# Kernel tuning notes

Measured on AMD Instinct MI355X. Metric: run time of the kernel, lower is better.

Reference implementation:

```python
import jax, jax.numpy as jnp
import numpy as np

T, B, DIN, DH, NH = 256, 256, 1024, 1024, 16
HD = DH // NH


def setup_inputs() -> dict:
    key = jax.random.key(0)
    ks = jax.random.split(key, 11)
    w = lambda k, shape: jax.random.normal(k, shape, jnp.float32) * 0.02
    return {
        "inputs": jax.random.normal(ks[0], (T, B, DIN), jnp.float32),
        "Wg": w(ks[1], (4, DIN + DH, DH)),  # forget, input, update, output pre-gate linears
        "bg": w(ks[2], (4, DH)),
        "Wq": w(ks[3], (3, DH, DH)),  # forget, input, output attention gates
        "bq": w(ks[4], (3, DH)),
        "Wk": w(ks[5], (3, DH, DH)),
        "bk": w(ks[6], (3, DH)),
        "Wv": w(ks[7], (3, DH, DH)),
        "bv": w(ks[8], (3, DH)),
        "Wo": w(ks[9], (3, DH, DH)),
        "bo": w(ks[10], (3, DH)),
    }


def reference(inputs, Wg, bg, Wq, bq, Wk, bk, Wv, bv, Wo, bo):
    scale = 1.0 / np.sqrt(HD)
    sel = jnp.array([0, 1, 3])  # gates that use attention: forget, input, output

    def attn_gate(x):
        # x: [3, B, DH] -- three gate pre-activations processed in parallel
        q = (jnp.einsum('gbd,gde->gbe', x, Wq) + bq[:, None, :]).reshape(3, B, NH, HD)
        k = (jnp.einsum('gbd,gde->gbe', x, Wk) + bk[:, None, :]).reshape(3, B, NH, HD)
        v = (jnp.einsum('gbd,gde->gbe', x, Wv) + bv[:, None, :]).reshape(3, B, NH, HD)
        # attention ACROSS heads: [3, B, NH, NH]
        aw = jax.nn.softmax(jnp.einsum('gbhd,gbkd->gbhk', q, k) * scale, axis=-1)
        ao = jnp.einsum('gbhk,gbkd->gbhd', aw, v).reshape(3, B, DH)
        return jax.nn.sigmoid(jnp.einsum('gbd,gde->gbe', ao, Wo) + bo[:, None, :])

    def step(carry, x):
        hx, cx = carry
        comb = jnp.concatenate([x, hx], axis=1)          # [B, DIN+DH]
        pre = jnp.einsum('bi,gio->gbo', comb, Wg) + bg[:, None, :]  # [4, B, DH]
        f, i, o = attn_gate(pre[sel])                    # each [B, DH]
        g = jnp.tanh(pre[2])
        cx = f * cx + i * g
        hx = o * jnp.tanh(cx)
        return (hx, cx), hx

    init = (jnp.zeros((B, DH), inputs.dtype), jnp.zeros((B, DH), inputs.dtype))
    (hx, cx), outputs = jax.lax.scan(step, init, inputs)
    return outputs, hx, cx
```

## Files before the change

kernel.cpp:

```cpp
#include <hip/hip_runtime.h>

typedef __attribute__((ext_vector_type(8))) short bf8;
typedef __attribute__((ext_vector_type(8))) unsigned short us8;
typedef __attribute__((ext_vector_type(4))) unsigned short us4;
typedef __attribute__((ext_vector_type(4))) float f4;

#define NB 256
#define OUT_HX_OFF ((size_t)256 * 256 * 1024)
#define OUT_CX_OFF (OUT_HX_OFF + (size_t)256 * 1024)

static __device__ __forceinline__ unsigned short f2bf(float f) {
    unsigned u = __builtin_bit_cast(unsigned, f);
    return (unsigned short)((u + 0x7FFFu + ((u >> 16) & 1u)) >> 16);
}
static __device__ __forceinline__ float bf2f(unsigned short h) {
    return __builtin_bit_cast(float, (unsigned)h << 16);
}
static __device__ __forceinline__ float sigm(float x) {
    return 1.0f / (1.0f + __expf(-x));
}

#define MFMA16(a, b, c) __builtin_amdgcn_mfma_f32_16x16x32_bf16(a, b, c, 0, 0, 0)

#define GLDS16(g, l)                                                        \
    __builtin_amdgcn_global_load_lds(                                       \
        (const __attribute__((address_space(1))) void*)(g),                 \
        (__attribute__((address_space(3))) void*)(l), 16, 0, 0)

#define WAITV(n) asm volatile("s_waitcnt vmcnt(" #n ")" ::: "memory")
#define WAITL0 asm volatile("s_waitcnt lgkmcnt(0)" ::: "memory")
#define BARRIER                                                             \
    do {                                                                    \
        __builtin_amdgcn_s_barrier();                                       \
        __builtin_amdgcn_sched_barrier(0);                                  \
    } while (0)

template <int R>
static __device__ __forceinline__ void stage64(const unsigned short* g, int gstride,
                                               unsigned short* lds, int wave, int lane) {
#pragma unroll
    for (int j = 0; j < R / 32; ++j) {
        const int seg = wave * (R / 32) + j;
        const int row = seg * 8 + (lane >> 3);
        const int chunk = (lane & 7) ^ (row & 7);
        GLDS16(g + (size_t)row * gstride + chunk * 8, lds + seg * 512);
    }
}

static __device__ __forceinline__ bf8 fragld(const unsigned short* lds, int row, int ck) {
    return *(const bf8*)&lds[row * 64 + (((ck) ^ (row & 7)) << 3)];
}

__global__ __launch_bounds__(256) void k_x2bf(const float* __restrict__ src,
                                              unsigned short* __restrict__ dst, int n4) {
    const int stride = gridDim.x * 256;
    for (int i = blockIdx.x * 256 + threadIdx.x; i < n4; i += stride) {
        f4 v = ((const f4*)src)[i];
        us4 o;
        o[0] = f2bf(v[0]); o[1] = f2bf(v[1]); o[2] = f2bf(v[2]); o[3] = f2bf(v[3]);
        ((us4*)dst)[i] = o;
    }
}

__global__ __launch_bounds__(256) void k_transpose(const float* __restrict__ src,
                                                   unsigned short* __restrict__ dst,
                                                   int K, int N) {
    __shared__ float tile[32][33];
    const int tx = threadIdx.x & 31, ty = threadIdx.x >> 5;
    const int n0 = blockIdx.x * 32, k0 = blockIdx.y * 32;
#pragma unroll
    for (int i = 0; i < 4; ++i) tile[ty + i * 8][tx] = src[(size_t)(k0 + ty + i * 8) * N + n0 + tx];
    __syncthreads();
#pragma unroll
    for (int i = 0; i < 4; ++i)
        dst[(size_t)(n0 + ty + i * 8) * K + k0 + tx] = f2bf(tile[tx][ty + i * 8]);
}

__global__ __launch_bounds__(256) void k_wfz(const unsigned short* __restrict__ wqkvT,
                                             const unsigned short* __restrict__ wgnt,
                                             unsigned short* __restrict__ wbigX,
                                             unsigned short* __restrict__ wbigH) {
    __shared__ unsigned short sA[2][128 * 64];
    __shared__ unsigned short sB[2][128 * 64];
    const int tid = threadIdx.x, lane = tid & 63, wave = tid >> 6;
    const int z = blockIdx.z, j = z >> 1, xh = z & 1;
    const int gp = j / 3, which = j % 3;
    const int selg = (gp == 2) ? 3 : gp;
    const unsigned short* Aab = wqkvT + ((size_t)gp * 3072 + which * 1024) * 1024;
    const unsigned short* Bb = wgnt + (size_t)selg * 2048 * 1024 + (size_t)xh * 1024 * 1024;
    unsigned short* outp = (xh ? wbigH : wbigX) + (size_t)j * 1024 * 1024;
    const int n0 = blockIdx.x * 128, m0 = blockIdx.y * 128;
    const int wy = (wave >> 1) * 64, wx = (wave & 1) * 64;
    const int fr = lane & 15, fq = lane >> 4;
    f4 acc[4][4] = {};

    stage64<128>(Aab + (size_t)m0 * 1024, 1024, sA[0], wave, lane);
    stage64<128>(Bb + (size_t)n0 * 1024, 1024, sB[0], wave, lane);
    WAITV(0); BARRIER;
#pragma unroll
    for (int i = 0; i < 16; ++i) {
        if (i + 1 < 16) {
            stage64<128>(Aab + (size_t)m0 * 1024 + (i + 1) * 64, 1024, sA[(i + 1) & 1], wave, lane);
            stage64<128>(Bb + (size_t)n0 * 1024 + (i + 1) * 64, 1024, sB[(i + 1) & 1], wave, lane);
        }
        const unsigned short* A = sA[i & 1];
        const unsigned short* Bm = sB[i & 1];
#pragma unroll
        for (int ks = 0; ks < 2; ++ks) {
            bf8 af[4], bfv[4];
#pragma unroll
            for (int mi = 0; mi < 4; ++mi) af[mi] = fragld(A, wy + mi * 16 + fr, ks * 4 + fq);
#pragma unroll
            for (int ni = 0; ni < 4; ++ni) bfv[ni] = fragld(Bm, wx + ni * 16 + fr, ks * 4 + fq);
#pragma unroll
            for (int mi = 0; mi < 4; ++mi)
#pragma unroll
                for (int ni = 0; ni < 4; ++ni)
                    acc[mi][ni] = MFMA16(af[mi], bfv[ni], acc[mi][ni]);
        }
        if (i + 1 < 16) { WAITL0; WAITV(0); BARRIER; }
    }
#pragma unroll
    for (int mi = 0; mi < 4; ++mi)
#pragma unroll
        for (int ni = 0; ni < 4; ++ni) {
            const int col = n0 + wx + ni * 16 + fr;
#pragma unroll
            for (int j2 = 0; j2 < 4; ++j2) {
                const int row = m0 + wy + mi * 16 + fq * 4 + j2;
                outp[(size_t)row * 1024 + col] = f2bf(acc[mi][ni][j2]);
            }
        }
}

__global__ __launch_bounds__(256) void k_seg9(const unsigned short* __restrict__ wgT,
                                              unsigned short* __restrict__ wbigX,
                                              unsigned short* __restrict__ wbigH) {
    const int d = blockIdx.x, k4 = threadIdx.x * 4;
    us4 vx = *(const us4*)(wgT + (size_t)(2048 + d) * 2048 + k4);
    us4 vh = *(const us4*)(wgT + (size_t)(2048 + d) * 2048 + 1024 + k4);
    *(us4*)(wbigX + (size_t)(9216 + d) * 1024 + k4) = vx;
    *(us4*)(wbigH + (size_t)(9216 + d) * 1024 + k4) = vh;
}

__global__ __launch_bounds__(256) void k_cbig(const float* __restrict__ bg,
                                              const float* __restrict__ Wq,
                                              const float* __restrict__ Wk,
                                              const float* __restrict__ Wv,
                                              const float* __restrict__ bq,
                                              const float* __restrict__ bk,
                                              const float* __restrict__ bv,
                                              float* __restrict__ cbig) {
    const int n = blockIdx.x * 256 + threadIdx.x;
    const int j = n >> 10, d = n & 1023;
    float s;
    if (j < 9) {
        const int gp = j / 3, which = j % 3;
        const int selg = (gp == 2) ? 3 : gp;
        const float* W = which == 0 ? Wq : (which == 1 ? Wk : Wv);
        const float* bqkv = which == 0 ? bq : (which == 1 ? bk : bv);
        s = bqkv[gp * 1024 + d];
        const float* wb = W + (size_t)gp * 1024 * 1024;
        const float* bgb = bg + selg * 1024;
        for (int k = 0; k < 1024; ++k) s += bgb[k] * wb[(size_t)k * 1024 + d];
    } else {
        s = bg[2048 + d];
    }
    cbig[n] = s;
}

__global__ __launch_bounds__(256) void k_xbig(const unsigned short* __restrict__ xbf,
                                              const unsigned short* __restrict__ wbigX,
                                              const float* __restrict__ cbig,
                                              unsigned short* __restrict__ XBIG) {
    __shared__ unsigned short sA[2][128 * 64];
    __shared__ unsigned short sB[2][128 * 64];
    const int tid = threadIdx.x, lane = tid & 63, wave = tid >> 6;
    const int n0 = blockIdx.x * 128;
    const size_t m0 = (size_t)blockIdx.y * 128;
    const int wy = (wave >> 1) * 64, wx = (wave & 1) * 64;
    const int fr = lane & 15, fq = lane >> 4;
    f4 acc[4][4] = {};

    stage64<128>(xbf + m0 * 1024, 1024, sA[0], wave, lane);
    stage64<128>(wbigX + (size_t)n0 * 1024, 1024, sB[0], wave, lane);
    WAITV(0); BARRIER;
#pragma unroll
    for (int i = 0; i < 16; ++i) {
        if (i + 1 < 16) {
            stage64<128>(xbf + m0 * 1024 + (i + 1) * 64, 1024, sA[(i + 1) & 1], wave, lane);
            stage64<128>(wbigX + (size_t)n0 * 1024 + (i + 1) * 64, 1024, sB[(i + 1) & 1], wave, lane);
        }
        const unsigned short* A = sA[i & 1];
        const unsigned short* Bm = sB[i & 1];
#pragma unroll
        for (int ks = 0; ks < 2; ++ks) {
            bf8 af[4], bfv[4];
#pragma unroll
            for (int mi = 0; mi < 4; ++mi) af[mi] = fragld(A, wy + mi * 16 + fr, ks * 4 + fq);
#pragma unroll
            for (int ni = 0; ni < 4; ++ni) bfv[ni] = fragld(Bm, wx + ni * 16 + fr, ks * 4 + fq);
#pragma unroll
            for (int mi = 0; mi < 4; ++mi)
#pragma unroll
                for (int ni = 0; ni < 4; ++ni)
                    acc[mi][ni] = MFMA16(af[mi], bfv[ni], acc[mi][ni]);
        }
        if (i + 1 < 16) { WAITL0; WAITV(0); BARRIER; }
    }
#pragma unroll
    for (int mi = 0; mi < 4; ++mi)
#pragma unroll
        for (int ni = 0; ni < 4; ++ni) {
            const int col = n0 + wx + ni * 16 + fr;
            const float b = cbig[col];
#pragma unroll
            for (int j = 0; j < 4; ++j) {
                const size_t row = m0 + wy + mi * 16 + fq * 4 + j;
                XBIG[row * 10240 + col] = f2bf(acc[mi][ni][j] + b);
            }
        }
}

__global__ __launch_bounds__(256, 3) void k_qg(
    const unsigned short* __restrict__ hxbf,
    const unsigned short* __restrict__ wbigH,
    const unsigned short* __restrict__ XBIGt,
    unsigned short* __restrict__ qkvbf,
    float* __restrict__ gupd) {
    __shared__ unsigned short sA[4][32 * 64];
    __shared__ unsigned short sB[4][64 * 64];
    const int tid = threadIdx.x, lane = tid & 63, wave = tid >> 6;
    const int n0 = blockIdx.x * 64, b0 = blockIdx.y * 32;
    const unsigned short* Aab = hxbf + (size_t)b0 * 1024;
    const unsigned short* Bb = wbigH + (size_t)n0 * 1024;
    const int wr = (wave & 1) * 16, wc = (wave >> 1) * 32;
    const int fr = lane & 15, fq = lane >> 4;
    f4 acc[2] = {};

#pragma unroll
    for (int p = 0; p < 3; ++p) {
        stage64<32>(Aab + p * 64, 1024, sA[p], wave, lane);
        stage64<64>(Bb + p * 64, 1024, sB[p], wave, lane);
    }
    WAITV(6); BARRIER;
#pragma unroll
    for (int i = 0; i < 16; ++i) {
        if (i + 3 < 16) {
            stage64<32>(Aab + (i + 3) * 64, 1024, sA[(i + 3) & 3], wave, lane);
            stage64<64>(Bb + (i + 3) * 64, 1024, sB[(i + 3) & 3], wave, lane);
        }
        const unsigned short* A = sA[i & 3];
        const unsigned short* Bm = sB[i & 3];
#pragma unroll
        for (int ks = 0; ks < 2; ++ks) {
            bf8 a0 = fragld(A, wr + fr, ks * 4 + fq);
            bf8 b0v = fragld(Bm, wc + fr, ks * 4 + fq);
            bf8 b1v = fragld(Bm, wc + 16 + fr, ks * 4 + fq);
            acc[0] = MFMA16(a0, b0v, acc[0]);
            acc[1] = MFMA16(a0, b1v, acc[1]);
        }
        if (i < 15) {
            WAITL0;
            if (i + 3 < 16) { WAITV(6); }
            else if (i + 2 < 16) { WAITV(3); }
            else { WAITV(0); }
            BARRIER;
        }
    }
#pragma unroll
    for (int ni = 0; ni < 2; ++ni) {
        const int col = n0 + wc + ni * 16 + fr;
        const int seg = col >> 10, d = col & 1023;
#pragma unroll
        for (int j = 0; j < 4; ++j) {
            const int row = b0 + wr + fq * 4 + j;
            const float v = acc[ni][j] + bf2f(XBIGt[(size_t)row * 10240 + col]);
            if (seg == 9) {
                gupd[(size_t)row * 1024 + d] = tanhf(v);
            } else {
                const int gp = seg / 3, which = seg % 3;
                qkvbf[((size_t)gp * NB + row) * 3072 + which * 1024 + d] = f2bf(v);
            }
        }
    }
}

__global__ __launch_bounds__(256, 2) void k_pre(
    const unsigned short* __restrict__ hxbf,
    const unsigned short* __restrict__ xt,
    const unsigned short* __restrict__ wgT,
    const float* __restrict__ bg,
    unsigned short* __restrict__ prebf,
    float* __restrict__ gupd) {
    __shared__ unsigned short sA[4][32 * 64];
    __shared__ unsigned short sB[4][64 * 64];
    const int tid = threadIdx.x, lane = tid & 63, wave = tid >> 6;
    const int n0 = blockIdx.x * 64, b0 = blockIdx.y * 32;
    const int wr = (wave & 1) * 16, wc = (wave >> 1) * 32;
    const int fr = lane & 15, fq = lane >> 4;
    constexpr int NT = 32;
    f4 acc[2] = {};

    const unsigned short* hb = hxbf + (size_t)b0 * 1024;
    const unsigned short* xb = xt + (size_t)b0 * 1024;
    auto asrc = [&](int i) -> const unsigned short* {
        return i < 16 ? xb + i * 64 : hb + (i - 16) * 64;
    };
    auto bsrc = [&](int i) -> const unsigned short* {
        return wgT + (size_t)n0 * 2048 + i * 64;
    };

#pragma unroll
    for (int p = 0; p < 3; ++p) {
        stage64<32>(asrc(p), 1024, sA[p], wave, lane);
        stage64<64>(bsrc(p), 2048, sB[p], wave, lane);
    }
    WAITV(6); BARRIER;
#pragma unroll
    for (int i = 0; i < NT; ++i) {
        if (i + 3 < NT) {
            stage64<32>(asrc(i + 3), 1024, sA[(i + 3) & 3], wave, lane);
            stage64<64>(bsrc(i + 3), 2048, sB[(i + 3) & 3], wave, lane);
        }
        const unsigned short* A = sA[i & 3];
        const unsigned short* Bm = sB[i & 3];
#pragma unroll
        for (int ks = 0; ks < 2; ++ks) {
            bf8 a0 = fragld(A, wr + fr, ks * 4 + fq);
            bf8 b0v = fragld(Bm, wc + fr, ks * 4 + fq);
            bf8 b1v = fragld(Bm, wc + 16 + fr, ks * 4 + fq);
            acc[0] = MFMA16(a0, b0v, acc[0]);
            acc[1] = MFMA16(a0, b1v, acc[1]);
        }
        if (i < NT - 1) {
            WAITL0;
            if (i + 3 < NT) { WAITV(6); }
            else if (i + 2 < NT) { WAITV(3); }
            else { WAITV(0); }
            BARRIER;
        }
    }
#pragma unroll
    for (int ni = 0; ni < 2; ++ni) {
        const int col = n0 + wc + ni * 16 + fr;
        const int gg = col >> 10, d = col & 1023;
#pragma unroll
        for (int j = 0; j < 4; ++j) {
            const int row = b0 + wr + fq * 4 + j;
            float v = acc[ni][j] + bg[col];
            if (gg == 2) {
                gupd[(size_t)row * 1024 + d] = tanhf(v);
            } else {
                const int gm = (gg == 3) ? 2 : gg;
                prebf[((size_t)gm * NB + row) * 1024 + d] = f2bf(v);
            }
        }
    }
}

__global__ __launch_bounds__(256, 3) void k_qkv(
    const unsigned short* __restrict__ prebf,
    const unsigned short* __restrict__ wqkvT,
    const float* __restrict__ bq,
    const float* __restrict__ bk,
    const float* __restrict__ bv,
    unsigned short* __restrict__ qkvbf) {
    __shared__ unsigned short sA[4][32 * 64];
    __shared__ unsigned short sB[4][64 * 64];
    const int tid = threadIdx.x, lane = tid & 63, wave = tid >> 6;
    const int g = blockIdx.z;
    const int n0 = blockIdx.x * 64, b0 = blockIdx.y * 32;
    const unsigned short* Aab = prebf + ((size_t)g * NB + b0) * 1024;
    const unsigned short* Bb = wqkvT + ((size_t)g * 3072 + n0) * 1024;
    const int wr = (wave & 1) * 16, wc = (wave >> 1) * 32;
    const int fr = lane & 15, fq = lane >> 4;
    f4 acc[2] = {};

#pragma unroll
    for (int p = 0; p < 3; ++p) {
        stage64<32>(Aab + p * 64, 1024, sA[p], wave, lane);
        stage64<64>(Bb + p * 64, 1024, sB[p], wave, lane);
    }
    WAITV(6); BARRIER;
#pragma unroll
    for (int i = 0; i < 16; ++i) {
        if (i + 3 < 16) {
            stage64<32>(Aab + (i + 3) * 64, 1024, sA[(i + 3) & 3], wave, lane);
            stage64<64>(Bb + (i + 3) * 64, 1024, sB[(i + 3) & 3], wave, lane);
        }
        const unsigned short* A = sA[i & 3];
        const unsigned short* Bm = sB[i & 3];
#pragma unroll
        for (int ks = 0; ks < 2; ++ks) {
            bf8 a0 = fragld(A, wr + fr, ks * 4 + fq);
            bf8 b0v = fragld(Bm, wc + fr, ks * 4 + fq);
            bf8 b1v = fragld(Bm, wc + 16 + fr, ks * 4 + fq);
            acc[0] = MFMA16(a0, b0v, acc[0]);
            acc[1] = MFMA16(a0, b1v, acc[1]);
        }
        if (i < 15) {
            WAITL0;
            if (i + 3 < 16) { WAITV(6); }
            else if (i + 2 < 16) { WAITV(3); }
            else { WAITV(0); }
            BARRIER;
        }
    }
#pragma unroll
    for (int ni = 0; ni < 2; ++ni) {
        const int col = n0 + wc + ni * 16 + fr;
        const int which = col >> 10, d = col & 1023;
        const float* bp = which == 0 ? bq : (which == 1 ? bk : bv);
        const float bias = bp[g * 1024 + d];
#pragma unroll
        for (int j = 0; j < 4; ++j) {
            const int row = b0 + wr + fq * 4 + j;
            qkvbf[((size_t)g * NB + row) * 3072 + col] = f2bf(acc[ni][j] + bias);
        }
    }
}

__global__ __launch_bounds__(256) void k_attn(const unsigned short* __restrict__ qkvbf,
                                              unsigned short* __restrict__ aobf) {
    __shared__ unsigned short qs[16][72], ksm[16][72], vsm[16][72];
    __shared__ float aw[16][17];
    const int b = blockIdx.x, g = blockIdx.y, tid = threadIdx.x;
    const unsigned short* src = qkvbf + ((size_t)g * NB + b) * 3072;
#pragma unroll
    for (int j = 0; j < 3; ++j) {
        const int n = (j * 256 + tid) * 4;
        us4 dv = *(const us4*)(src + n);
        const int part = n >> 10, h = (n >> 6) & 15, c = n & 63;
        unsigned short* dst = part == 0 ? &qs[h][c] : (part == 1 ? &ksm[h][c] : &vsm[h][c]);
        *(us4*)dst = dv;
    }
    __syncthreads();
    const int h = tid >> 4, kp = tid & 15;
    float s = 0.f;
#pragma unroll
    for (int dblk = 0; dblk < 8; ++dblk) {
        us8 qv = *(const us8*)&qs[h][dblk * 8];
        us8 kv = *(const us8*)&ksm[kp][dblk * 8];
#pragma unroll
        for (int e = 0; e < 8; ++e) s += bf2f(qv[e]) * bf2f(kv[e]);
    }
    s *= 0.125f;
    float m = s;
#pragma unroll
    for (int off = 8; off; off >>= 1) m = fmaxf(m, __shfl_xor(m, off, 16));
    const float p = __expf(s - m);
    float sum = p;
#pragma unroll
    for (int off = 8; off; off >>= 1) sum += __shfl_xor(sum, off, 16);
    aw[h][kp] = p / sum;
    __syncthreads();
    float a0 = 0.f, a1 = 0.f, a2 = 0.f, a3 = 0.f;
#pragma unroll
    for (int kk = 0; kk < 16; ++kk) {
        const float w = aw[h][kk];
        us4 vv = *(const us4*)&vsm[kk][kp * 4];
        a0 += w * bf2f(vv[0]); a1 += w * bf2f(vv[1]);
        a2 += w * bf2f(vv[2]); a3 += w * bf2f(vv[3]);
    }
    us4 ov;
    ov[0] = f2bf(a0); ov[1] = f2bf(a1); ov[2] = f2bf(a2); ov[3] = f2bf(a3);
    *(us4*)(aobf + ((size_t)g * NB + b) * 1024 + h * 64 + kp * 4) = ov;
}

__global__ __launch_bounds__(256, 1) void k_gate(
    const unsigned short* __restrict__ aobf,
    const unsigned short* __restrict__ woT,
    const float* __restrict__ bo,
    const float* __restrict__ gupd,
    unsigned short* __restrict__ hxbf,
    float* __restrict__ out, int t) {
    __shared__ unsigned short sA[4][3][32 * 64];
    __shared__ unsigned short sB[4][3][32 * 64];
    const int tid = threadIdx.x, lane = tid & 63, wave = tid >> 6;
    const int d0 = blockIdx.x * 32, b0 = blockIdx.y * 32;
    const int wr = (wave & 1) * 16, wc = (wave >> 1) * 16;
    const int fr = lane & 15, fq = lane >> 4;
    f4 acc[3] = {};

    auto stage_all = [&](int i, int slot) {
#pragma unroll
        for (int g = 0; g < 3; ++g) {
            stage64<32>(aobf + ((size_t)g * NB + b0) * 1024 + i * 64, 1024,
                        sA[slot][g], wave, lane);
            stage64<32>(woT + ((size_t)g * 1024 + d0) * 1024 + i * 64, 1024,
                        sB[slot][g], wave, lane);
        }
    };

    stage_all(0, 0);
    stage_all(1, 1);
    stage_all(2, 2);
    WAITV(12); BARRIER;
#pragma unroll
    for (int i = 0; i < 16; ++i) {
        if (i + 3 < 16) stage_all(i + 3, (i + 3) & 3);
        const int sl = i & 3;
#pragma unroll
        for (int g = 0; g < 3; ++g) {
#pragma unroll
            for (int ks = 0; ks < 2; ++ks) {
                bf8 a0 = fragld(sA[sl][g], wr + fr, ks * 4 + fq);
                bf8 b0v = fragld(sB[sl][g], wc + fr, ks * 4 + fq);
                acc[g] = MFMA16(a0, b0v, acc[g]);
            }
        }
        if (i < 15) {
            WAITL0;
            if (i + 3 < 16) { WAITV(12); }
            else if (i + 2 < 16) { WAITV(6); }
            else { WAITV(0); }
            BARRIER;
        }
    }

    const int col = d0 + wc + fr;
    const float bof = bo[col], boi = bo[1024 + col], boo = bo[2048 + col];
    float* cxp = out + OUT_CX_OFF;
    float* hxp = out + OUT_HX_OFF;
    float* outs = out + (size_t)t * NB * 1024;
#pragma unroll
    for (int j = 0; j < 4; ++j) {
        const int row = b0 + wr + fq * 4 + j;
        const size_t idx = (size_t)row * 1024 + col;
        const float fg = sigm(acc[0][j] + bof);
        const float ig = sigm(acc[1][j] + boi);
        const float og = sigm(acc[2][j] + boo);
        const float c = fg * cxp[idx] + ig * gupd[idx];
        const float h = og * tanhf(c);
        cxp[idx] = c;
        hxp[idx] = h;
        outs[idx] = h;
        hxbf[idx] = f2bf(h);
    }
}

extern "C" void kernel_launch(void* const* d_in, const int* in_sizes, int n_in,
                              void* d_out, int out_size, void* d_ws, size_t ws_size,
                              hipStream_t stream) {
    const float* inputs = (const float*)d_in[0];
    const float* Wg = (const float*)d_in[1];
    const float* bg = (const float*)d_in[2];
    const float* Wq = (const float*)d_in[3];
    const float* bq = (const float*)d_in[4];
    const float* Wk = (const float*)d_in[5];
    const float* bk = (const float*)d_in[6];
    const float* Wv = (const float*)d_in[7];
    const float* bv = (const float*)d_in[8];
    const float* Wo = (const float*)d_in[9];
    const float* bo = (const float*)d_in[10];
    float* out = (float*)d_out;
    (void)in_sizes; (void)n_in; (void)out_size;

    char* ws = (char*)d_ws;
    size_t off = 0;
    auto alloc = [&](size_t bytes) -> void* {
        void* p = ws + off;
        off += (bytes + 255) & ~(size_t)255;
        return p;
    };
    unsigned short* wgT   = (unsigned short*)alloc((size_t)4096 * 2048 * 2);
    unsigned short* wqkvT = (unsigned short*)alloc((size_t)3 * 3072 * 1024 * 2);
    unsigned short* woT   = (unsigned short*)alloc((size_t)3 * 1024 * 1024 * 2);
    unsigned short* wgnt  = (unsigned short*)alloc((size_t)4 * 2048 * 1024 * 2);
    unsigned short* hxbf  = (unsigned short*)alloc((size_t)256 * 1024 * 2);
    unsigned short* prebf = (unsigned short*)alloc((size_t)3 * 256 * 1024 * 2);
    float*          gupd  = (float*)alloc((size_t)256 * 1024 * 4);
    unsigned short* qkvbf = (unsigned short*)alloc((size_t)3 * 256 * 3072 * 2);
    unsigned short* aobf  = (unsigned short*)alloc((size_t)3 * 256 * 1024 * 2);
    unsigned short* xbfs  = (unsigned short*)alloc((size_t)2 * 256 * 1024 * 2);
    const size_t off_base = off;
    unsigned short* xbf   = (unsigned short*)alloc((size_t)65536 * 1024 * 2);
    const size_t off_xbf = off;
    unsigned short* wbigX = (unsigned short*)alloc((size_t)10240 * 1024 * 2);
    unsigned short* wbigH = (unsigned short*)alloc((size_t)10240 * 1024 * 2);
    float*          cbig  = (float*)alloc((size_t)10240 * 4);
    const size_t off_wb = off;
    unsigned short* XBIGc = (unsigned short*)(ws + off_wb);

    int CH = 0;
    for (int c = 64; c >= 4; c >>= 1) {
        if (ws_size >= off_wb + (size_t)c * 256 * 10240 * 2) { CH = c; break; }
    }
    int tier;
    if (CH > 0) tier = 0;
    else if (ws_size >= off_xbf) tier = 2;
    else if (ws_size >= off_base) tier = 3;
    else return;

    hipMemsetAsync(hxbf, 0, (size_t)256 * 1024 * 2, stream);
    hipMemsetAsync(out + OUT_CX_OFF, 0, (size_t)256 * 1024 * 4, stream);

    for (int g = 0; g < 4; ++g)
        k_transpose<<<dim3(32, 64), 256, 0, stream>>>(
            Wg + (size_t)g * 2048 * 1024, wgT + (size_t)g * 1024 * 2048, 2048, 1024);
    const float* wsrc[3] = {Wq, Wk, Wv};
    for (int g = 0; g < 3; ++g)
        for (int wi = 0; wi < 3; ++wi)
            k_transpose<<<dim3(32, 32), 256, 0, stream>>>(
                wsrc[wi] + (size_t)g * 1024 * 1024,
                wqkvT + (size_t)g * 3072 * 1024 + (size_t)wi * 1024 * 1024, 1024, 1024);
    for (int g = 0; g < 3; ++g)
        k_transpose<<<dim3(32, 32), 256, 0, stream>>>(
            Wo + (size_t)g * 1024 * 1024, woT + (size_t)g * 1024 * 1024, 1024, 1024);

    if (tier <= 2) k_x2bf<<<2048, 256, 0, stream>>>(inputs, xbf, 16777216);

    if (tier == 0) {
        k_x2bf<<<2048, 256, 0, stream>>>(Wg, wgnt, 2097152);
        k_wfz<<<dim3(8, 8, 18), 256, 0, stream>>>(wqkvT, wgnt, wbigX, wbigH);
        k_seg9<<<1024, 256, 0, stream>>>(wgT, wbigX, wbigH);
        k_cbig<<<40, 256, 0, stream>>>(bg, Wq, Wk, Wv, bq, bk, bv, cbig);

        for (int c = 0; c < 256 / CH; ++c) {
            k_xbig<<<dim3(80, CH * 2), 256, 0, stream>>>(
                xbf + (size_t)c * CH * 256 * 1024, wbigX, cbig, XBIGc);
            for (int tl = 0; tl < CH; ++tl) {
                const int t = c * CH + tl;
                k_qg<<<dim3(160, 8), 256, 0, stream>>>(
                    hxbf, wbigH, XBIGc + (size_t)tl * 256 * 10240, qkvbf, gupd);
                k_attn<<<dim3(256, 3), 256, 0, stream>>>(qkvbf, aobf);
                k_gate<<<dim3(32, 8), 256, 0, stream>>>(aobf, woT, bo, gupd, hxbf, out, t);
            }
        }
    } else {
        for (int t = 0; t < 256; ++t) {
            if (tier == 3)
                k_x2bf<<<64, 256, 0, stream>>>(inputs + (size_t)t * 262144,
                                               xbfs + (size_t)(t & 1) * 262144, 65536);
            k_pre<<<dim3(64, 8), 256, 0, stream>>>(
                hxbf,
                tier == 2 ? xbf + (size_t)t * 262144 : xbfs + (size_t)(t & 1) * 262144,
                wgT, bg, prebf, gupd);
            k_qkv<<<dim3(48, 8, 3), 256, 0, stream>>>(prebf, wqkvT, bq, bk, bv, qkvbf);
            k_attn<<<dim3(256, 3), 256, 0, stream>>>(qkvbf, aobf);
            k_gate<<<dim3(32, 8), 256, 0, stream>>>(aobf, woT, bo, gupd, hxbf, out, t);
        }
    }
}
```

Measured before the change: 12.89 ms.

## Replace LDS-staged pipelines with direct global fragment loads in recurrent GEMM kernels

Removes the shared-memory staging buffers, multi-stage async copy pipeline and barriers from k_qg, k_qkv and k_gate. Each wave now loads its MFMA operand fragments straight from global memory, relying on L2/L1 for reuse, and occupancy hints are raised to 4 blocks per CU. The aim is to cut barrier and LDS overhead in these small latency-bound per-timestep GEMMs. The cost is redundant global loads across waves, with no explicit prefetch left to hide memory latency.

Result: slower. 24.94 ms (+93.5%).

```diff
diff --git a/kernel.cpp b/kernel.cpp
--- a/kernel.cpp
+++ b/kernel.cpp
@@ -222,51 +222,29 @@
         }
 }
 
-__global__ __launch_bounds__(256, 3) void k_qg(
+__global__ __launch_bounds__(256, 4) void k_qg(
     const unsigned short* __restrict__ hxbf,
     const unsigned short* __restrict__ wbigH,
     const unsigned short* __restrict__ XBIGt,
     unsigned short* __restrict__ qkvbf,
     float* __restrict__ gupd) {
-    __shared__ unsigned short sA[4][32 * 64];
-    __shared__ unsigned short sB[4][64 * 64];
     const int tid = threadIdx.x, lane = tid & 63, wave = tid >> 6;
     const int n0 = blockIdx.x * 64, b0 = blockIdx.y * 32;
-    const unsigned short* Aab = hxbf + (size_t)b0 * 1024;
-    const unsigned short* Bb = wbigH + (size_t)n0 * 1024;
     const int wr = (wave & 1) * 16, wc = (wave >> 1) * 32;
     const int fr = lane & 15, fq = lane >> 4;
     f4 acc[2] = {};
 
-#pragma unroll
-    for (int p = 0; p < 3; ++p) {
-        stage64<32>(Aab + p * 64, 1024, sA[p], wave, lane);
-        stage64<64>(Bb + p * 64, 1024, sB[p], wave, lane);
-    }
-    WAITV(6); BARRIER;
-#pragma unroll
-    for (int i = 0; i < 16; ++i) {
-        if (i + 3 < 16) {
-            stage64<32>(Aab + (i + 3) * 64, 1024, sA[(i + 3) & 3], wave, lane);
-            stage64<64>(Bb + (i + 3) * 64, 1024, sB[(i + 3) & 3], wave, lane);
-        }
-        const unsigned short* A = sA[i & 3];
-        const unsigned short* Bm = sB[i & 3];
-#pragma unroll
-        for (int ks = 0; ks < 2; ++ks) {
-            bf8 a0 = fragld(A, wr + fr, ks * 4 + fq);
-            bf8 b0v = fragld(Bm, wc + fr, ks * 4 + fq);
-            bf8 b1v = fragld(Bm, wc + 16 + fr, ks * 4 + fq);
-            acc[0] = MFMA16(a0, b0v, acc[0]);
-            acc[1] = MFMA16(a0, b1v, acc[1]);
-        }
-        if (i < 15) {
-            WAITL0;
-            if (i + 3 < 16) { WAITV(6); }
-            else if (i + 2 < 16) { WAITV(3); }
-            else { WAITV(0); }
-            BARRIER;
-        }
+    const unsigned short* arow = hxbf + (size_t)(b0 + wr + fr) * 1024 + fq * 8;
+    const unsigned short* brow0 = wbigH + (size_t)(n0 + wc + fr) * 1024 + fq * 8;
+    const unsigned short* brow1 = wbigH + (size_t)(n0 + wc + 16 + fr) * 1024 + fq * 8;
+#pragma unroll
+    for (int i = 0; i < 32; ++i) {
+        const int ko = i * 32;
+        bf8 a0 = *(const bf8*)(arow + ko);
+        bf8 b0v = *(const bf8*)(brow0 + ko);
+        bf8 b1v = *(const bf8*)(brow1 + ko);
+        acc[0] = MFMA16(a0, b0v, acc[0]);
+        acc[1] = MFMA16(a0, b1v, acc[1]);
     }
 #pragma unroll
     for (int ni = 0; ni < 2; ++ni) {
@@ -359,53 +337,31 @@
     }
 }
 
-__global__ __launch_bounds__(256, 3) void k_qkv(
+__global__ __launch_bounds__(256, 4) void k_qkv(
     const unsigned short* __restrict__ prebf,
     const unsigned short* __restrict__ wqkvT,
     const float* __restrict__ bq,
     const float* __restrict__ bk,
     const float* __restrict__ bv,
     unsigned short* __restrict__ qkvbf) {
-    __shared__ unsigned short sA[4][32 * 64];
-    __shared__ unsigned short sB[4][64 * 64];
     const int tid = threadIdx.x, lane = tid & 63, wave = tid >> 6;
     const int g = blockIdx.z;
     const int n0 = blockIdx.x * 64, b0 = blockIdx.y * 32;
-    const unsigned short* Aab = prebf + ((size_t)g * NB + b0) * 1024;
-    const unsigned short* Bb = wqkvT + ((size_t)g * 3072 + n0) * 1024;
     const int wr = (wave & 1) * 16, wc = (wave >> 1) * 32;
     const int fr = lane & 15, fq = lane >> 4;
     f4 acc[2] = {};
 
-#pragma unroll
-    for (int p = 0; p < 3; ++p) {
-        stage64<32>(Aab + p * 64, 1024, sA[p], wave, lane);
-        stage64<64>(Bb + p * 64, 1024, sB[p], wave, lane);
-    }
-    WAITV(6); BARRIER;
-#pragma unroll
-    for (int i = 0; i < 16; ++i) {
-        if (i + 3 < 16) {
-            stage64<32>(Aab + (i + 3) * 64, 1024, sA[(i + 3) & 3], wave, lane);
-            stage64<64>(Bb + (i + 3) * 64, 1024, sB[(i + 3) & 3], wave, lane);
-        }
-        const unsigned short* A = sA[i & 3];
-        const unsigned short* Bm = sB[i & 3];
-#pragma unroll
-        for (int ks = 0; ks < 2; ++ks) {
-            bf8 a0 = fragld(A, wr + fr, ks * 4 + fq);
-            bf8 b0v = fragld(Bm, wc + fr, ks * 4 + fq);
-            bf8 b1v = fragld(Bm, wc + 16 + fr, ks * 4 + fq);
-            acc[0] = MFMA16(a0, b0v, acc[0]);
-            acc[1] = MFMA16(a0, b1v, acc[1]);
-        }
-        if (i < 15) {
-            WAITL0;
-            if (i + 3 < 16) { WAITV(6); }
-            else if (i + 2 < 16) { WAITV(3); }
-            else { WAITV(0); }
-            BARRIER;
-        }
+    const unsigned short* arow = prebf + ((size_t)g * NB + b0 + wr + fr) * 1024 + fq * 8;
+    const unsigned short* brow0 = wqkvT + ((size_t)g * 3072 + n0 + wc + fr) * 1024 + fq * 8;
+    const unsigned short* brow1 = wqkvT + ((size_t)g * 3072 + n0 + wc + 16 + fr) * 1024 + fq * 8;
+#pragma unroll
+    for (int i = 0; i < 32; ++i) {
+        const int ko = i * 32;
+        bf8 a0 = *(const bf8*)(arow + ko);
+        bf8 b0v = *(const bf8*)(brow0 + ko);
+        bf8 b1v = *(const bf8*)(brow1 + ko);
+        acc[0] = MFMA16(a0, b0v, acc[0]);
+        acc[1] = MFMA16(a0, b1v, acc[1]);
     }
 #pragma unroll
     for (int ni = 0; ni < 2; ++ni) {
@@ -468,55 +424,31 @@
     *(us4*)(aobf + ((size_t)g * NB + b) * 1024 + h * 64 + kp * 4) = ov;
 }
 
-__global__ __launch_bounds__(256, 1) void k_gate(
+__global__ __launch_bounds__(256, 4) void k_gate(
     const unsigned short* __restrict__ aobf,
     const unsigned short* __restrict__ woT,
     const float* __restrict__ bo,
     const float* __restrict__ gupd,
     unsigned short* __restrict__ hxbf,
     float* __restrict__ out, int t) {
-    __shared__ unsigned short sA[4][3][32 * 64];
-    __shared__ unsigned short sB[4][3][32 * 64];
     const int tid = threadIdx.x, lane = tid & 63, wave = tid >> 6;
     const int d0 = blockIdx.x * 32, b0 = blockIdx.y * 32;
     const int wr = (wave & 1) * 16, wc = (wave >> 1) * 16;
     const int fr = lane & 15, fq = lane >> 4;
     f4 acc[3] = {};
 
-    auto stage_all = [&](int i, int slot) {
-#pragma unroll
-        for (int g = 0; g < 3; ++g) {
-            stage64<32>(aobf + ((size_t)g * NB + b0) * 1024 + i * 64, 1024,
-                        sA[slot][g], wave, lane);
-            stage64<32>(woT + ((size_t)g * 1024 + d0) * 1024 + i * 64, 1024,
-                        sB[slot][g], wave, lane);
-        }
-    };
-
-    stage_all(0, 0);
-    stage_all(1, 1);
-    stage_all(2, 2);
-    WAITV(12); BARRIER;
-#pragma unroll
-    for (int i = 0; i < 16; ++i) {
-        if (i + 3 < 16) stage_all(i + 3, (i + 3) & 3);
-        const int sl = i & 3;
-#pragma unroll
-        for (int g = 0; g < 3; ++g) {
-#pragma unroll
-            for (int ks = 0; ks < 2; ++ks) {
-                bf8 a0 = fragld(sA[sl][g], wr + fr, ks * 4 + fq);
-                bf8 b0v = fragld(sB[sl][g], wc + fr, ks * 4 + fq);
-                acc[g] = MFMA16(a0, b0v, acc[g]);
-            }
-        }
-        if (i < 15) {
-            WAITL0;
-            if (i + 3 < 16) { WAITV(12); }
-            else if (i + 2 < 16) { WAITV(6); }
-            else { WAITV(0); }
-            BARRIER;
-        }
+    const unsigned short* ar0 = aobf + ((size_t)0 * NB + b0 + wr + fr) * 1024 + fq * 8;
+    const unsigned short* ar1 = aobf + ((size_t)1 * NB + b0 + wr + fr) * 1024 + fq * 8;
+    const unsigned short* ar2 = aobf + ((size_t)2 * NB + b0 + wr + fr) * 1024 + fq * 8;
+    const unsigned short* br0 = woT + ((size_t)0 * 1024 + d0 + wc + fr) * 1024 + fq * 8;
+    const unsigned short* br1 = woT + ((size_t)1 * 1024 + d0 + wc + fr) * 1024 + fq * 8;
+    const unsigned short* br2 = woT + ((size_t)2 * 1024 + d0 + wc + fr) * 1024 + fq * 8;
+#pragma unroll
+    for (int i = 0; i < 32; ++i) {
+        const int ko = i * 32;
+        acc[0] = MFMA16(*(const bf8*)(ar0 + ko), *(const bf8*)(br0 + ko), acc[0]);
+        acc[1] = MFMA16(*(const bf8*)(ar1 + ko), *(const bf8*)(br1 + ko), acc[1]);
+        acc[2] = MFMA16(*(const bf8*)(ar2 + ko), *(const bf8*)(br2 + ko), acc[2]);
     }
 
     const int col = d0 + wc + fr;
```
